# Optimization experiments

Hardware: AMD Instinct MI355X
Metric: run time of the kernel (lower is better)

## Reference

```python
import jax, jax.numpy as jnp
import numpy as np

B, N, D, H = 4, 2048, 768, 12
HD = D // H
SCALE = HD ** -0.5


def setup_inputs() -> dict:
    key = jax.random.key(0)
    k1, k2, k3 = jax.random.split(key, 3)
    x = jax.random.normal(k1, (B, N, D), dtype=jnp.float32)
    w_qkv = jax.random.normal(k2, (D, 3 * D), dtype=jnp.float32) * (D ** -0.5)
    w_proj = jax.random.normal(k3, (D, D), dtype=jnp.float32) * (D ** -0.5)
    b_proj = jnp.zeros((D,), dtype=jnp.float32)
    return {"x": x, "w_qkv": w_qkv, "w_proj": w_proj, "b_proj": b_proj}


def reference(x, w_qkv, w_proj, b_proj):
    b, n, d = x.shape
    qkv = x @ w_qkv                      # [b, n, 3d]
    q, k, v = jnp.split(qkv, 3, axis=-1)
    # [b, n, d] -> [b, h, n, hd]
    split_heads = lambda t: t.reshape(b, n, H, HD).transpose(0, 2, 1, 3)
    q, k, v = split_heads(q), split_heads(k), split_heads(v)
    dots = jnp.einsum('bhqd,bhkd->bhqk', q, k) * SCALE   # [b, h, n, n]
    attn = jax.nn.softmax(dots, axis=-1)
    q_attn = attn[:, :, 0, :]            # attention row of query token 0: [b, h, n]
    # dropout p=0 (eval) -> identity
    out = jnp.einsum('bhqk,bhkd->bhqd', attn, v)          # [b, h, n, hd]
    out = out.transpose(0, 2, 1, 3).reshape(b, n, d)      # [b, n, d]
    return out @ w_proj + b_proj, q_attn
```

## Files before the change

kernel.cpp:

```cpp
#include <hip/hip_runtime.h>


typedef unsigned short u16;
typedef __attribute__((ext_vector_type(8))) short bf8;
typedef __attribute__((ext_vector_type(4))) short bf4;
typedef __attribute__((ext_vector_type(4))) int i4;
typedef __attribute__((ext_vector_type(4))) float f4;

#define MFMA16(a, b, c) __builtin_amdgcn_mfma_f32_16x16x32_bf16((a), (b), (c), 0, 0, 0)

#if __has_builtin(__builtin_amdgcn_exp2f)
#define EXP2(x) __builtin_amdgcn_exp2f(x)
#else
#define EXP2(x) __expf((x) * 0.6931471805599453f)
#endif

__device__ __forceinline__ float b2f(u16 h) {
  union { unsigned u; float f; } v; v.u = ((unsigned)h) << 16; return v.f;
}
__device__ __forceinline__ u16 f2b(float f) {
  union { float f; unsigned u; } v; v.f = f;
  unsigned r = v.u + 0x7fffu + ((v.u >> 16) & 1u);
  return (u16)(r >> 16);
}
__device__ __forceinline__ unsigned pack2(float a, float b) {
#if __has_builtin(__builtin_amdgcn_perm)
  return __builtin_amdgcn_perm(__builtin_bit_cast(unsigned, b),
                               __builtin_bit_cast(unsigned, a), 0x07060302u);
#else
  return (__builtin_bit_cast(unsigned, b) & 0xFFFF0000u) |
         (__builtin_bit_cast(unsigned, a) >> 16);
#endif
}
__device__ __forceinline__ void gload16(const u16* g, u16* l) {
  __builtin_amdgcn_global_load_lds(
      (const __attribute__((address_space(1))) void*)g,
      (__attribute__((address_space(3))) void*)l, 16, 0, 0);
}
__device__ __forceinline__ int detect_f32(const u16* x) {
  unsigned v = x[2 * (threadIdx.x & 63)];
  unsigned e = (v >> 7) & 0xFF;
  return __ballot(e >= 0x8E) != 0ull;
}

__global__ __launch_bounds__(256) void prep(
    const void* __restrict__ x, u16* __restrict__ xbf,
    const void* __restrict__ wqkv, u16* __restrict__ wqkvT,
    const void* __restrict__ wproj, u16* __restrict__ wprojT) {
  const int z = blockIdx.z;
  if (z == 2) {
    const int f32 = detect_f32((const u16*)x);
    const int lin = blockIdx.y * 72 + blockIdx.x;
    if (f32) {
      const float2* in = (const float2*)x;
      unsigned* out = (unsigned*)xbf;
      for (int i = lin * 256 + threadIdx.x; i < 3145728; i += 442368) {
        float2 v = in[i];
        out[i] = (unsigned)f2b(v.x) | ((unsigned)f2b(v.y) << 16);
      }
    } else {
      const unsigned* in = (const unsigned*)x;
      unsigned* out = (unsigned*)xbf;
      for (int i = lin * 256 + threadIdx.x; i < 3145728; i += 442368)
        out[i] = in[i];
    }
    return;
  }
  if (z == 1 && blockIdx.x >= 24) return;
  const void* in = z ? wproj : wqkv;
  u16* out = z ? wprojT : wqkvT;
  const int R = 768, C = z ? 768 : 2304;
  __shared__ u16 tile[32][33];
  const int f32 = detect_f32((const u16*)x);
  const int bx = blockIdx.x * 32, by = blockIdx.y * 32;
  const int tx = threadIdx.x & 31, ty = threadIdx.x >> 5;
#pragma unroll
  for (int i = 0; i < 4; i++) {
    size_t idx = (size_t)(by + ty + i * 8) * C + bx + tx;
    tile[ty + i * 8][tx] = f32 ? f2b(((const float*)in)[idx]) : ((const u16*)in)[idx];
  }
  __syncthreads();
#pragma unroll
  for (int i = 0; i < 4; i++)
    out[(size_t)(bx + ty + i * 8) * R + by + tx] = tile[tx][ty + i * 8];
}

__global__ __launch_bounds__(512, 4) void gemm_qkv8(
    const u16* __restrict__ A, const u16* __restrict__ Bt,
    u16* __restrict__ Cq, u16* __restrict__ Vt) {
  __shared__ alignas(16) u16 L[3][13312];
  const int t = threadIdx.x;
  const int lane = t & 63, wave = t >> 6;
  const int wr = wave >> 1, wc = wave & 1;
  const int quad = lane >> 4, l16 = lane & 15;
  const int bm = blockIdx.y * 128, bn = blockIdx.x * 288;
  const int dcol = ((lane & 3) ^ ((lane >> 3) & 3)) * 8;
  const int swzU = (quad ^ ((l16 >> 1) & 3)) * 8;
  const int drow = lane >> 2;
  f4 acc[2][9] = {};

#define STAGE(kt, buf)                                                       \
  {                                                                          \
    _Pragma("unroll")                                                        \
    for (int s = 0; s < 4; s++) {                                            \
      int c = wave + s * 8;                                                  \
      if (c >= 26) c = wave;            \
      const int isB = c >= 8;                                                \
      const int rb = isB ? c - 8 : c;                                        \
      const u16* src = (isB ? Bt : A) +                                      \
          (size_t)((isB ? bn : bm) + rb * 16 + drow) * 768 +                 \
          (kt) * 32 + dcol;                                                  \
      u16* dst = &L[buf][(isB ? 4096 : 0) + rb * 512];                       \
      gload16(src, dst);                                                     \
    }                                                                        \
  }

  STAGE(0, 0);
  STAGE(1, 1);

  int cur = 0;
  for (int j = 0; j < 24; j++) {
    if (j < 23) {
      asm volatile("s_waitcnt vmcnt(4)" ::: "memory");
    } else {
      asm volatile("s_waitcnt vmcnt(0)" ::: "memory");
    }
    __builtin_amdgcn_s_barrier();
    if (j + 2 < 24) {
      int pre = cur + 2; if (pre >= 3) pre -= 3;
      STAGE(j + 2, pre);
    }
    const u16* Lb = &L[cur][0];
    bf8 af[2];
#pragma unroll
    for (int m = 0; m < 2; m++)
      af[m] = *(const bf8*)&Lb[(wr * 32 + m * 16 + l16) * 32 + swzU];
#pragma unroll
    for (int p = 0; p < 3; p++) {
      bf8 bfr[3];
#pragma unroll
      for (int nn = 0; nn < 3; nn++)
        bfr[nn] = *(const bf8*)&Lb[4096 +
            (wc * 144 + (p * 3 + nn) * 16 + l16) * 32 + swzU];
      __builtin_amdgcn_s_setprio(1);
#pragma unroll
      for (int nn = 0; nn < 3; nn++)
#pragma unroll
        for (int m = 0; m < 2; m++)
          acc[m][p * 3 + nn] = MFMA16(af[m], bfr[nn], acc[m][p * 3 + nn]);
      __builtin_amdgcn_s_setprio(0);
    }
    cur = (cur == 2) ? 0 : cur + 1;
  }
#undef STAGE

  const int b_ = bm >> 11;
#pragma unroll
  for (int m = 0; m < 2; m++) {
    const int row0 = bm + wr * 32 + m * 16 + quad * 4;
    const int n0 = row0 & 2047;
    const int n2 = (n0 & ~31) | (((n0 >> 2) & 3) << 3) | (((n0 >> 4) & 1) << 2);
#pragma unroll
    for (int ni = 0; ni < 9; ni++) {
      const int col = bn + wc * 144 + ni * 16 + l16;
      if (col >= 1536) {
        const int colv = col - 1536, h = colv >> 6, d = colv & 63;
        bf4 pk = {(short)f2b(acc[m][ni][0]), (short)f2b(acc[m][ni][1]),
                  (short)f2b(acc[m][ni][2]), (short)f2b(acc[m][ni][3])};
        *(bf4*)&Vt[(size_t)((b_ * 12 + h) * 64 + d) * 2048 + n2] = pk;
      } else {
#pragma unroll
        for (int r = 0; r < 4; r++)
          Cq[(size_t)(row0 + r) * 2304 + col] = f2b(acc[m][ni][r]);
      }
    }
  }
}

__global__ __launch_bounds__(256, 3) void gemm_proj4(
    const u16* __restrict__ A, const u16* __restrict__ Bt,
    const void* __restrict__ bias, void* __restrict__ C,
    const u16* __restrict__ xdet, const float* __restrict__ qe,
    const float* __restrict__ lout) {
  if (blockIdx.x == 6) {
    if (blockIdx.y >= 64) return;
    const int f32o = detect_f32(xdet);
    const int base = blockIdx.y * 1536;
    for (int j = threadIdx.x; j < 1536; j += 256) {
      int idx = base + j;
      float v = qe[idx] * (1.f / lout[idx >> 11]);
      size_t oidx = (size_t)6291456 + idx;
      if (f32o) ((float*)C)[oidx] = v; else ((u16*)C)[oidx] = f2b(v);
    }
    return;
  }
  __shared__ alignas(16) u16 L[3][6144];
  const int t = threadIdx.x;
  const int lane = t & 63, wave = t >> 6;
  const int wr = wave >> 1, wc = wave & 1;
  const int quad = lane >> 4, l16 = lane & 15;
  const int bm = blockIdx.y * 64, bn = blockIdx.x * 128;
  const int f32o = detect_f32(xdet);
  const int dcol = ((lane & 3) ^ ((lane >> 3) & 3)) * 8;
  const int swzU = (quad ^ ((l16 >> 1) & 3)) * 8;
  const int drow = lane >> 2;
  f4 acc[2][4] = {};

#define STAGE(kt, buf)                                                       \
  {                                                                          \
    _Pragma("unroll")                                                        \
    for (int s = 0; s < 3; s++) {                                            \
      const int c = wave + s * 4;                                            \
      const int isB = c >= 4;                                                \
      const int rb = isB ? c - 4 : c;                                        \
      const u16* src = (isB ? Bt : A) +                                      \
          (size_t)((isB ? bn : bm) + rb * 16 + drow) * 768 +                 \
          (kt) * 32 + dcol;                                                  \
      u16* dst = &L[buf][(isB ? 2048 : 0) + rb * 512];                       \
      gload16(src, dst);                                                     \
    }                                                                        \
  }

  STAGE(0, 0);
  STAGE(1, 1);

  int cur = 0;
  for (int j = 0; j < 24; j++) {
    if (j < 23) {
      asm volatile("s_waitcnt vmcnt(3)" ::: "memory");
    } else {
      asm volatile("s_waitcnt vmcnt(0)" ::: "memory");
    }
    __builtin_amdgcn_s_barrier();
    if (j + 2 < 24) {
      int pre = cur + 2; if (pre >= 3) pre -= 3;
      STAGE(j + 2, pre);
    }
    const u16* Lb = &L[cur][0];
    bf8 af[2], bfr[4];
#pragma unroll
    for (int m = 0; m < 2; m++)
      af[m] = *(const bf8*)&Lb[(wr * 32 + m * 16 + l16) * 32 + swzU];
#pragma unroll
    for (int nt = 0; nt < 4; nt++)
      bfr[nt] = *(const bf8*)&Lb[2048 + (wc * 64 + nt * 16 + l16) * 32 + swzU];
    __builtin_amdgcn_s_setprio(1);
#pragma unroll
    for (int nt = 0; nt < 4; nt++)
#pragma unroll
      for (int m = 0; m < 2; m++)
        acc[m][nt] = MFMA16(af[m], bfr[nt], acc[m][nt]);
    __builtin_amdgcn_s_setprio(0);
    cur = (cur == 2) ? 0 : cur + 1;
  }
#undef STAGE

#pragma unroll
  for (int m = 0; m < 2; m++) {
    const int row0 = bm + wr * 32 + m * 16 + quad * 4;
#pragma unroll
    for (int nt = 0; nt < 4; nt++) {
      const int col = bn + wc * 64 + nt * 16 + l16;
      const float bv = f32o ? ((const float*)bias)[col]
                            : b2f(((const u16*)bias)[col]);
#pragma unroll
      for (int r = 0; r < 4; r++) {
        size_t idx = (size_t)(row0 + r) * 768 + col;
        float v = acc[m][nt][r] + bv;
        if (f32o) ((float*)C)[idx] = v; else ((u16*)C)[idx] = f2b(v);
      }
    }
  }
}

template <int BIAS, int QATTN>
__global__ __launch_bounds__(256, 4) void gemm_bt(
    const u16* __restrict__ A, const u16* __restrict__ Bt,
    const void* __restrict__ bias, void* __restrict__ C,
    int M, int Ncols, int K, const u16* __restrict__ xdet,
    u16* __restrict__ Vt, const float* __restrict__ qe,
    const float* __restrict__ lout) {
  if (QATTN && blockIdx.x == 6) {
    const int f32o = detect_f32(xdet);
    const int base = blockIdx.y * 1536;
    for (int j = threadIdx.x; j < 1536; j += 256) {
      int idx = base + j;
      float v = qe[idx] * (1.f / lout[idx >> 11]);
      size_t oidx = (size_t)6291456 + idx;
      if (f32o) ((float*)C)[oidx] = v; else ((u16*)C)[oidx] = f2b(v);
    }
    return;
  }
  __shared__ alignas(16) u16 Al[2][128 * 32];
  __shared__ alignas(16) u16 Bl[2][128 * 32];
  const int t = threadIdx.x;
  const int lane = t & 63, wave = t >> 6;
  const int wr = wave >> 1, wc = wave & 1;
  const int quad = lane >> 4, l16 = lane & 15;
  const int bm = blockIdx.y * 128, bn = blockIdx.x * 128;
  const int f32o = BIAS ? detect_f32(xdet) : 0;
  const int grow = lane >> 2, gcol = (lane & 3) * 8;
  const int chunk0 = wave * 2, chunk1 = wave * 2 + 1;
  const int arow0 = chunk0 * 16 + grow, arow1 = chunk1 * 16 + grow;
  f4 acc[4][4] = {};
  gload16(A + (size_t)(bm + arow0) * K + gcol, &Al[0][chunk0 * 512]);
  gload16(Bt + (size_t)(bn + arow0) * K + gcol, &Bl[0][chunk0 * 512]);
  gload16(A + (size_t)(bm + arow1) * K + gcol, &Al[0][chunk1 * 512]);
  gload16(Bt + (size_t)(bn + arow1) * K + gcol, &Bl[0][chunk1 * 512]);
  const int NIT = K >> 5;
  for (int i = 0; i < NIT; i++) {
    const int cur = i & 1, nxt = cur ^ 1;
    __syncthreads();
    if (i + 1 < NIT) {
      int k0 = (i + 1) << 5;
      gload16(A + (size_t)(bm + arow0) * K + k0 + gcol, &Al[nxt][chunk0 * 512]);
      gload16(Bt + (size_t)(bn + arow0) * K + k0 + gcol, &Bl[nxt][chunk0 * 512]);
      gload16(A + (size_t)(bm + arow1) * K + k0 + gcol, &Al[nxt][chunk1 * 512]);
      gload16(Bt + (size_t)(bn + arow1) * K + k0 + gcol, &Bl[nxt][chunk1 * 512]);
    }
    bf8 af[4], bfr[4];
#pragma unroll
    for (int mt = 0; mt < 4; mt++)
      af[mt] = *(const bf8*)&Al[cur][(wr * 64 + mt * 16 + l16) * 32 + quad * 8];
#pragma unroll
    for (int nt = 0; nt < 4; nt++)
      bfr[nt] = *(const bf8*)&Bl[cur][(wc * 64 + nt * 16 + l16) * 32 + quad * 8];
#pragma unroll
    for (int mt = 0; mt < 4; mt++)
#pragma unroll
      for (int nt = 0; nt < 4; nt++)
        acc[mt][nt] = MFMA16(af[mt], bfr[nt], acc[mt][nt]);
  }
  if (Vt != nullptr && bn >= 1536) {
    const int b = bm >> 11;
#pragma unroll
    for (int mt = 0; mt < 4; mt++) {
      int n0 = (bm & 2047) + wr * 64 + mt * 16 + quad * 4;
      int n2 = (n0 & ~31) | (((n0 >> 2) & 3) << 3) | (((n0 >> 4) & 1) << 2);
#pragma unroll
      for (int nt = 0; nt < 4; nt++) {
        int colv = bn - 1536 + wc * 64 + nt * 16 + l16;
        int h = colv >> 6, d = colv & 63;
        bf4 pk = {(short)f2b(acc[mt][nt][0]), (short)f2b(acc[mt][nt][1]),
                  (short)f2b(acc[mt][nt][2]), (short)f2b(acc[mt][nt][3])};
        *(bf4*)&Vt[(size_t)((b * 12 + h) * 64 + d) * 2048 + n2] = pk;
      }
    }
    return;
  }
#pragma unroll
  for (int mt = 0; mt < 4; mt++) {
    int row = bm + wr * 64 + mt * 16 + quad * 4;
#pragma unroll
    for (int nt = 0; nt < 4; nt++) {
      int col = bn + wc * 64 + nt * 16 + l16;
      float bv = 0.f;
      if (BIAS)
        bv = f32o ? ((const float*)bias)[col] : b2f(((const u16*)bias)[col]);
#pragma unroll
      for (int r = 0; r < 4; r++) {
        size_t idx = (size_t)(row + r) * Ncols + col;
        float v = acc[mt][nt][r] + bv;
        if (f32o) ((float*)C)[idx] = v; else ((u16*)C)[idx] = f2b(v);
      }
    }
  }
}

__global__ __launch_bounds__(256, 3) void flash_attn(
    const u16* __restrict__ qkv, const u16* __restrict__ Vt,
    u16* __restrict__ O, float* __restrict__ qe, float* __restrict__ lout) {
  __shared__ alignas(16) u16 lds[3][8192];
  const int t = threadIdx.x, lane = t & 63, wave = t >> 6;
  const int quad = lane >> 4, l16 = lane & 15;
  const int id = blockIdx.x;
  const int bh = (id & 7) + 8 * (id >> 7);
  const int qtile = (id >> 3) & 15;
  const int b = bh / 12, h = bh - b * 12;
  const int q0 = qtile * 128 + wave * 32;
  const bool dumpP = (qe != nullptr) && (qtile == 0) && (wave == 0);
  const float SCALE2 = 0.125f * 1.44269504089f;
  const float mM0 = -16.f;
  bf8 qf[2][2];
#pragma unroll
  for (int qt = 0; qt < 2; qt++) {
    const u16* Qr = qkv + (size_t)(b * 2048 + q0 + qt * 16 + l16) * 2304 + h * 64;
    bf8 r0 = *(const bf8*)(Qr + quad * 8);
    bf8 r1 = *(const bf8*)(Qr + 32 + quad * 8);
#pragma unroll
    for (int j = 0; j < 8; j++) {
      qf[qt][0][j] = (short)f2b(b2f((u16)r0[j]) * SCALE2);
      qf[qt][1][j] = (short)f2b(b2f((u16)r1[j]) * SCALE2);
    }
  }
  bf8 ones;
#pragma unroll
  for (int j = 0; j < 8; j++) ones[j] = (short)0x3F80;
  const u16* Kb = qkv + (size_t)(b * 2048) * 2304 + 768 + h * 64;
  const u16* Vb = Vt + (size_t)((b * 12 + h) * 64) * 2048;
  const int drow = wave * 16 + (lane >> 2);
  const int dcol = ((lane & 3) ^ ((lane >> 3) & 3)) * 8;
  const int swz = (quad ^ ((l16 >> 1) & 3)) * 8;
  f4 o[2][4] = {};
  f4 lacc[2] = {};

#define STAGE(tile, buf)                                            \
  {                                                                 \
    int n1_ = (tile) * 64;                                          \
    const u16* Kt_ = Kb + (size_t)(n1_ + drow) * 2304 + dcol;       \
    const u16* Vr_ = Vb + (size_t)drow * 2048 + n1_ + dcol;         \
    u16* base_ = &lds[buf][wave * 512];                             \
    gload16(Kt_, base_);                                            \
    gload16(Kt_ + 32, base_ + 2048);                                \
    gload16(Vr_, base_ + 4096);                                     \
    gload16(Vr_ + 32, base_ + 6144);                                \
  }

  STAGE(0, 0);
  STAGE(1, 1);

  int cur = 0;
  for (int i = 0; i < 32; i++) {
    if (i < 31) {
      asm volatile("s_waitcnt vmcnt(4)" ::: "memory");
    } else {
      asm volatile("s_waitcnt vmcnt(0)" ::: "memory");
    }
    __builtin_amdgcn_s_barrier();
    if (i + 2 < 32) {
      int pre = cur + 2; if (pre >= 3) pre -= 3;
      STAGE(i + 2, pre);
    }
    const u16* K0 = &lds[cur][0];
    const u16* K1 = &lds[cur][2048];
    union { i4 i; bf8 b; } pf[2][2];
#pragma unroll
    for (int kt = 0; kt < 4; kt++) {
      bf8 kf0 = *(const bf8*)&K0[(kt * 16 + l16) * 32 + swz];
      bf8 kf1 = *(const bf8*)&K1[(kt * 16 + l16) * 32 + swz];
#pragma unroll
      for (int qt = 0; qt < 2; qt++) {
        f4 z = {mM0, mM0, mM0, mM0};
        z = MFMA16(kf0, qf[qt][0], z);
        z = MFMA16(kf1, qf[qt][1], z);
        float e0 = EXP2(z[0]);
        float e1 = EXP2(z[1]);
        float e2 = EXP2(z[2]);
        float e3 = EXP2(z[3]);
        if (qt == 0 && dumpP && l16 == 0) {
          f4 ev = {e0, e1, e2, e3};
          *(f4*)&qe[bh * 2048 + i * 64 + kt * 16 + quad * 4] = ev;
        }
        pf[qt][kt >> 1].i[(kt & 1) * 2 + 0] = (int)pack2(e0, e1);
        pf[qt][kt >> 1].i[(kt & 1) * 2 + 1] = (int)pack2(e2, e3);
      }
    }
#pragma unroll
    for (int pair = 0; pair < 2; pair++) {
      const u16* Vp = &lds[cur][4096 + pair * 2048];
      lacc[0] = MFMA16(ones, pf[0][pair].b, lacc[0]);
      lacc[1] = MFMA16(ones, pf[1][pair].b, lacc[1]);
#pragma unroll
      for (int nt = 0; nt < 4; nt++) {
        bf8 vf = *(const bf8*)&Vp[(nt * 16 + l16) * 32 + swz];
        o[0][nt] = MFMA16(vf, pf[0][pair].b, o[0][nt]);
        o[1][nt] = MFMA16(vf, pf[1][pair].b, o[1][nt]);
      }
    }
    cur = (cur == 2) ? 0 : cur + 1;
  }
#undef STAGE
#pragma unroll
  for (int qt = 0; qt < 2; qt++) {
    float l = lacc[qt][0];
    if (qt == 0 && dumpP && lane == 0) lout[bh] = l;
    float inv = 1.f / l;
    size_t row = (size_t)(b * 2048 + q0 + qt * 16 + l16) * 768 + h * 64;
#pragma unroll
    for (int nt = 0; nt < 4; nt++) {
      bf4 pk = {(short)f2b(o[qt][nt][0] * inv), (short)f2b(o[qt][nt][1] * inv),
                (short)f2b(o[qt][nt][2] * inv), (short)f2b(o[qt][nt][3] * inv)};
      *(bf4*)&O[row + nt * 16 + quad * 4] = pk;
    }
  }
}

__global__ __launch_bounds__(256) void qattn_row0(
    const u16* __restrict__ qkv, void* __restrict__ out,
    const u16* __restrict__ xdet) {
  const int bh = blockIdx.x, b = bh / 12, h = bh % 12;
  __shared__ float qs[64];
  __shared__ float sv[2048];
  __shared__ float red[8];
  const int t = threadIdx.x;
  const int f32o = detect_f32(xdet);
  if (t < 64) qs[t] = b2f(qkv[(size_t)(b * 2048) * 2304 + h * 64 + t]);
  __syncthreads();
  float lmax = -1e30f;
  for (int k = t; k < 2048; k += 256) {
    const u16* Kr = qkv + (size_t)(b * 2048 + k) * 2304 + 768 + h * 64;
    float acc = 0.f;
#pragma unroll
    for (int j = 0; j < 8; j++) {
      bf8 kv = *(const bf8*)(Kr + j * 8);
#pragma unroll
      for (int d = 0; d < 8; d++) acc += qs[j * 8 + d] * b2f((u16)kv[d]);
    }
    acc *= 0.125f;
    sv[k] = acc;
    lmax = fmaxf(lmax, acc);
  }
#pragma unroll
  for (int off = 32; off >= 1; off >>= 1) lmax = fmaxf(lmax, __shfl_xor(lmax, off, 64));
  if ((t & 63) == 0) red[t >> 6] = lmax;
  __syncthreads();
  const float bmax = fmaxf(fmaxf(red[0], red[1]), fmaxf(red[2], red[3]));
  float lsum = 0.f;
  for (int k = t; k < 2048; k += 256) {
    float e = __expf(sv[k] - bmax);
    sv[k] = e;
    lsum += e;
  }
#pragma unroll
  for (int off = 32; off >= 1; off >>= 1) lsum += __shfl_xor(lsum, off, 64);
  if ((t & 63) == 0) red[4 + (t >> 6)] = lsum;
  __syncthreads();
  const float inv = 1.f / (red[4] + red[5] + red[6] + red[7]);
  for (int k = t; k < 2048; k += 256) {
    size_t idx = (size_t)6291456 + (size_t)bh * 2048 + k;
    float v = sv[k] * inv;
    if (f32o) ((float*)out)[idx] = v; else ((u16*)out)[idx] = f2b(v);
  }
}

extern "C" void kernel_launch(void* const* d_in, const int* in_sizes, int n_in,
                              void* d_out, int out_size, void* d_ws, size_t ws_size,
                              hipStream_t stream) {
  const void* x_raw      = d_in[0];
  const void* w_qkv_raw  = d_in[1];
  const void* w_proj_raw = d_in[2];
  const void* b_proj_raw = d_in[3];
  const u16* xdet = (const u16*)x_raw;
  char* ws = (char*)d_ws;
  u16* xbf    = (u16*)(ws + 256);
  u16* wqkvT  = (u16*)(ws + 12583168);
  u16* wprojT = (u16*)(ws + 16122112);
  u16* qkv    = (u16*)(ws + 17301760);
  u16* Vt     = (u16*)(ws + 55050496);
  float* qe   = (float*)(ws + 67633408);
  float* lout = (float*)(ws + 68026624);
  u16* attn   = xbf;
  const bool fused = ws_size >= 68026816ull;

  prep<<<dim3(72, 24, 3), 256, 0, stream>>>(
      x_raw, xbf, w_qkv_raw, wqkvT, w_proj_raw, wprojT);
  gemm_qkv8<<<dim3(8, 64), 512, 0, stream>>>(xbf, wqkvT, qkv, Vt);
  flash_attn<<<dim3(768), 256, 0, stream>>>(qkv, Vt, attn,
                                            fused ? qe : nullptr,
                                            fused ? lout : nullptr);
  if (fused) {
    gemm_proj4<<<dim3(7, 128), 256, 0, stream>>>(
        attn, wprojT, b_proj_raw, d_out, xdet, qe, lout);
  } else {
    gemm_bt<1, 0><<<dim3(6, 64), 256, 0, stream>>>(
        attn, wprojT, b_proj_raw, d_out, 8192, 768, 768, xdet, nullptr, nullptr, nullptr);
    qattn_row0<<<dim3(48), 256, 0, stream>>>(qkv, d_out, xdet);
  }
}
```

Measured before the change: 208.2 us.

## Transpose Q/K MFMA tiles for packed stores and split attention launch

In the QKV GEMM, the Q/K column fragments now compute the transposed MFMA product (B fragment first) so each lane holds four consecutive columns and can write a packed 8-byte bf16 store instead of four scattered 2-byte stores. V fragments keep the original orientation for the transposed Vt layout. Separately, the flash attention launch is split into two 384-block launches using an id offset, which adds a launch but may change scheduling or tail behaviour.

Result: slower. 231.4 us (+11.2%).

```diff
diff --git a/kernel.cpp b/kernel.cpp
--- a/kernel.cpp
+++ b/kernel.cpp
@@ -98,6 +98,10 @@
   const int swzU = (quad ^ ((l16 >> 1) & 3)) * 8;
   const int drow = lane >> 2;
   f4 acc[2][9] = {};
+  bool vfrag[9];
+#pragma unroll
+  for (int ni = 0; ni < 9; ni++)
+    vfrag[ni] = (bn + wc * 144 + ni * 16) >= 1536;
 
 #define STAGE(kt, buf)                                                       \
   {                                                                          \
@@ -146,8 +150,13 @@
 #pragma unroll
       for (int nn = 0; nn < 3; nn++)
 #pragma unroll
-        for (int m = 0; m < 2; m++)
-          acc[m][p * 3 + nn] = MFMA16(af[m], bfr[nn], acc[m][p * 3 + nn]);
+        for (int m = 0; m < 2; m++) {
+          const int ni = p * 3 + nn;
+          if (vfrag[ni])
+            acc[m][ni] = MFMA16(af[m], bfr[nn], acc[m][ni]);
+          else
+            acc[m][ni] = MFMA16(bfr[nn], af[m], acc[m][ni]);
+        }
       __builtin_amdgcn_s_setprio(0);
     }
     cur = (cur == 2) ? 0 : cur + 1;
@@ -157,21 +166,23 @@
   const int b_ = bm >> 11;
 #pragma unroll
   for (int m = 0; m < 2; m++) {
-    const int row0 = bm + wr * 32 + m * 16 + quad * 4;
-    const int n0 = row0 & 2047;
-    const int n2 = (n0 & ~31) | (((n0 >> 2) & 3) << 3) | (((n0 >> 4) & 1) << 2);
 #pragma unroll
     for (int ni = 0; ni < 9; ni++) {
-      const int col = bn + wc * 144 + ni * 16 + l16;
-      if (col >= 1536) {
+      if (vfrag[ni]) {
+        const int row0 = bm + wr * 32 + m * 16 + quad * 4;
+        const int n0 = row0 & 2047;
+        const int n2 = (n0 & ~31) | (((n0 >> 2) & 3) << 3) | (((n0 >> 4) & 1) << 2);
+        const int col = bn + wc * 144 + ni * 16 + l16;
         const int colv = col - 1536, h = colv >> 6, d = colv & 63;
         bf4 pk = {(short)f2b(acc[m][ni][0]), (short)f2b(acc[m][ni][1]),
                   (short)f2b(acc[m][ni][2]), (short)f2b(acc[m][ni][3])};
         *(bf4*)&Vt[(size_t)((b_ * 12 + h) * 64 + d) * 2048 + n2] = pk;
       } else {
-#pragma unroll
-        for (int r = 0; r < 4; r++)
-          Cq[(size_t)(row0 + r) * 2304 + col] = f2b(acc[m][ni][r]);
+        const int row = bm + wr * 32 + m * 16 + l16;
+        const int colq = bn + wc * 144 + ni * 16 + quad * 4;
+        bf4 pk = {(short)f2b(acc[m][ni][0]), (short)f2b(acc[m][ni][1]),
+                  (short)f2b(acc[m][ni][2]), (short)f2b(acc[m][ni][3])};
+        *(bf4*)&Cq[(size_t)row * 2304 + colq] = pk;
       }
     }
   }
@@ -369,11 +380,12 @@
 
 __global__ __launch_bounds__(256, 3) void flash_attn(
     const u16* __restrict__ qkv, const u16* __restrict__ Vt,
-    u16* __restrict__ O, float* __restrict__ qe, float* __restrict__ lout) {
+    u16* __restrict__ O, float* __restrict__ qe, float* __restrict__ lout,
+    int idbase) {
   __shared__ alignas(16) u16 lds[3][8192];
   const int t = threadIdx.x, lane = t & 63, wave = t >> 6;
   const int quad = lane >> 4, l16 = lane & 15;
-  const int id = blockIdx.x;
+  const int id = blockIdx.x + idbase;
   const int bh = (id & 7) + 8 * (id >> 7);
   const int qtile = (id >> 3) & 15;
   const int b = bh / 12, h = bh - b * 12;
@@ -555,9 +567,12 @@
   prep<<<dim3(72, 24, 3), 256, 0, stream>>>(
       x_raw, xbf, w_qkv_raw, wqkvT, w_proj_raw, wprojT);
   gemm_qkv8<<<dim3(8, 64), 512, 0, stream>>>(xbf, wqkvT, qkv, Vt);
-  flash_attn<<<dim3(768), 256, 0, stream>>>(qkv, Vt, attn,
+  flash_attn<<<dim3(384), 256, 0, stream>>>(qkv, Vt, attn,
                                             fused ? qe : nullptr,
-                                            fused ? lout : nullptr);
+                                            fused ? lout : nullptr, 0);
+  flash_attn<<<dim3(384), 256, 0, stream>>>(qkv, Vt, attn,
+                                            fused ? qe : nullptr,
+                                            fused ? lout : nullptr, 384);
   if (fused) {
     gemm_proj4<<<dim3(7, 128), 256, 0, stream>>>(
         attn, wprojT, b_proj_raw, d_out, xdet, qe, lout);
```
